# Kernel tuning notes

Measured on AMD Instinct MI355X. Metric: run time of the kernel, lower is better.

Reference implementation:

```python
import jax, jax.numpy as jnp
import numpy as np

STEPS = 2


def _gru_unit(adj, x, mask3, Wz0, Wz1, Wr0, Wr1, Wh0, Wh1, bz0, bz1, br0, br1, bh0, bh1):
    # adj: [B,N,N], x: [B,N,D], mask3: [B,N,1]
    a = jnp.einsum('bnm,bmd->bnd', adj, x)  # neighborhood aggregation
    z = jax.nn.sigmoid(a @ Wz0 + bz0 + x @ Wz1 + bz1)  # update gate
    r = jax.nn.sigmoid(a @ Wr0 + br0 + x @ Wr1 + br1)  # reset gate
    h = jax.nn.relu(mask3 * (a @ Wh0 + bh0 + (r * x) @ Wh1 + bh1))
    return h * z + x * (1.0 - z)


def setup_inputs() -> dict:
    key = jax.random.key(0)
    ks = jax.random.split(key, 10)
    B, N, Din, Dout = 256, 512, 300, 96

    def glorot(k, shape):
        lim = np.sqrt(6.0 / (shape[0] + shape[1]))
        return jax.random.uniform(k, shape, jnp.float32, -lim, lim)

    return {
        'x': jax.random.normal(ks[0], (B, N, Din), jnp.float32),
        'adj': jax.random.uniform(ks[1], (B, N, N), jnp.float32),
        'mask': jnp.ones((B, N), jnp.float32),
        'W_enc': glorot(ks[2], (Din, Dout)),
        'b_enc': jnp.zeros((Dout,), jnp.float32),
        'Wz0': glorot(ks[3], (Dout, Dout)),
        'Wz1': glorot(ks[4], (Dout, Dout)),
        'Wr0': glorot(ks[5], (Dout, Dout)),
        'Wr1': glorot(ks[6], (Dout, Dout)),
        'Wh0': glorot(ks[7], (Dout, Dout)),
        'Wh1': glorot(ks[8], (Dout, Dout)),
        'bz0': jnp.zeros((Dout,), jnp.float32),
        'bz1': jnp.zeros((Dout,), jnp.float32),
        'br0': jnp.zeros((Dout,), jnp.float32),
        'br1': jnp.zeros((Dout,), jnp.float32),
        'bh0': jnp.zeros((Dout,), jnp.float32),
        'bh1': jnp.zeros((Dout,), jnp.float32),
    }


def reference(x, adj, mask, W_enc, b_enc, Wz0, Wz1, Wr0, Wr1, Wh0, Wh1,
              bz0, bz1, br0, br1, bh0, bh1):
    mask3 = mask[..., None]                     # [B,N,1]
    xe = mask3 * jax.nn.relu(x)                 # dropout rate 0 -> identity
    out = xe @ W_enc + b_enc                    # [B,N,Dout]
    for _ in range(STEPS):
        out = _gru_unit(adj, out, mask3, Wz0, Wz1, Wr0, Wr1, Wh0, Wh1,
                        bz0, bz1, br0, br1, bh0, bh1)
    return out
```

## Files before the change

kernel.cpp:

```cpp
#include <hip/hip_runtime.h>

typedef short  bfrag  __attribute__((ext_vector_type(8)));
typedef float  facc4  __attribute__((ext_vector_type(4)));
typedef unsigned short u16;
typedef unsigned int   u32;

#define MROWS 131072
#define DD    96

__device__ __forceinline__ u16 f2b(float f) {
  u32 u = __float_as_uint(f);
  return (u16)((u + 0x7FFFu + ((u >> 16) & 1u)) >> 16);
}
__device__ __forceinline__ float b2f(u16 h) {
  return __uint_as_float(((u32)h) << 16);
}
__device__ __forceinline__ void splitf(float x, u16& h, u16& l) {
  h = f2b(x);
  l = f2b(x - b2f(h));
}
__device__ __forceinline__ void split4(float4 v, ushort4& oh, ushort4& ol) {
  splitf(v.x, oh.x, ol.x); splitf(v.y, oh.y, ol.y);
  splitf(v.z, oh.z, ol.z); splitf(v.w, oh.w, ol.w);
}

#define MFMA __builtin_amdgcn_mfma_f32_16x16x32_bf16

__global__ void k_prep(const float* __restrict__ Wenc,
                       const float* __restrict__ benc,
                       const float* __restrict__ Wz0, const float* __restrict__ Wz1,
                       const float* __restrict__ Wr0, const float* __restrict__ Wr1,
                       const float* __restrict__ Wh0, const float* __restrict__ Wh1,
                       const float* __restrict__ bz0, const float* __restrict__ bz1,
                       const float* __restrict__ br0, const float* __restrict__ br1,
                       const float* __restrict__ bh0, const float* __restrict__ bh1,
                       u16* __restrict__ wencTh, u16* __restrict__ wencTl,
                       u16* __restrict__ wzrTh,  u16* __restrict__ wzrTl,
                       u16* __restrict__ whTh,   u16* __restrict__ whTl,
                       float* __restrict__ bias)
{
  int i = blockIdx.x * 256 + threadIdx.x;
  if (i < 36864) {
    int n = i / 384, k = i % 384;
    float v = (k < 300) ? Wenc[k * 96 + n] : 0.f;
    u16 h, l; splitf(v, h, l);
    wencTh[i] = h; wencTl[i] = l;
  } else if (i < 73728) {
    int j = i - 36864;
    int g = j / 18432, r = j % 18432;
    int n = r / 192, k = r % 192;
    const float* W0 = g ? Wr0 : Wz0;
    const float* W1 = g ? Wr1 : Wz1;
    float v = (k < 96) ? W0[k * 96 + n] : W1[(k - 96) * 96 + n];
    u16 h, l; splitf(v, h, l);
    wzrTh[j] = h; wzrTl[j] = l;
  } else if (i < 92160) {
    int j = i - 73728;
    int n = j / 192, k = j % 192;
    float v = (k < 96) ? Wh0[k * 96 + n] : Wh1[(k - 96) * 96 + n];
    u16 h, l; splitf(v, h, l);
    whTh[j] = h; whTl[j] = l;
  } else if (i < 92544) {
    int j = i - 92160;
    int r = j / 96, n = j % 96;
    float v;
    if      (r == 0) v = benc[n];
    else if (r == 1) v = bz0[n] + bz1[n];
    else if (r == 2) v = br0[n] + br1[n];
    else             v = bh0[n] + bh1[n];
    bias[j] = v;
  }
}

__global__ __launch_bounds__(256) void k_enc(const float* __restrict__ x,
    const float* __restrict__ mask,
    const u16* __restrict__ wTh, const u16* __restrict__ wTl,
    const float* __restrict__ bias, float* __restrict__ xf)
{
  __shared__ u16 sAh[128][72], sAl[128][72];
  __shared__ u16 sBh[96][72],  sBl[96][72];
  const int tid = threadIdx.x;
  const int wave = tid >> 6, lane = tid & 63, q = lane >> 4, l15 = lane & 15;
  const int m0 = blockIdx.x * 128;
  facc4 acc[2][6] = {};
  for (int c = 0; c < 5; ++c) {
    int k0 = c * 64;
    {
      int rl = tid >> 2, cg = tid & 3;
      for (int it = 0; it < 2; ++it) {
        int row = rl + it * 64;
        int grow = m0 + row;
        float mk = mask[grow];
        const float* xr = x + (size_t)grow * 300 + k0;
        #pragma unroll
        for (int j = 0; j < 4; ++j) {
          int kk = (cg + j * 4) * 4;
          float4 v;
          if (k0 + kk + 4 <= 300) v = *(const float4*)(xr + kk);
          else                    v = make_float4(0.f, 0.f, 0.f, 0.f);
          v.x = fmaxf(v.x, 0.f) * mk; v.y = fmaxf(v.y, 0.f) * mk;
          v.z = fmaxf(v.z, 0.f) * mk; v.w = fmaxf(v.w, 0.f) * mk;
          ushort4 oh, ol; split4(v, oh, ol);
          *(ushort4*)&sAh[row][kk] = oh;
          *(ushort4*)&sAl[row][kk] = ol;
        }
      }
    }
    {
      for (int u = tid; u < 768; u += 256) {
        int n = u >> 3, kk = (u & 7) * 8;
        size_t off = (size_t)n * 384 + k0 + kk;
        *(uint4*)&sBh[n][kk] = *(const uint4*)(wTh + off);
        *(uint4*)&sBl[n][kk] = *(const uint4*)(wTl + off);
      }
    }
    __syncthreads();
    #pragma unroll
    for (int ks = 0; ks < 2; ++ks) {
      int kb = ks * 32 + q * 8;
      bfrag a0h = *(const bfrag*)&sAh[wave * 32 + l15][kb];
      bfrag a0l = *(const bfrag*)&sAl[wave * 32 + l15][kb];
      bfrag a1h = *(const bfrag*)&sAh[wave * 32 + 16 + l15][kb];
      bfrag a1l = *(const bfrag*)&sAl[wave * 32 + 16 + l15][kb];
      #pragma unroll
      for (int nt = 0; nt < 6; ++nt) {
        bfrag bh = *(const bfrag*)&sBh[nt * 16 + l15][kb];
        bfrag bl = *(const bfrag*)&sBl[nt * 16 + l15][kb];
        acc[0][nt] = MFMA(a0h, bh, acc[0][nt], 0, 0, 0);
        acc[0][nt] = MFMA(a0h, bl, acc[0][nt], 0, 0, 0);
        acc[0][nt] = MFMA(a0l, bh, acc[0][nt], 0, 0, 0);
        acc[1][nt] = MFMA(a1h, bh, acc[1][nt], 0, 0, 0);
        acc[1][nt] = MFMA(a1h, bl, acc[1][nt], 0, 0, 0);
        acc[1][nt] = MFMA(a1l, bh, acc[1][nt], 0, 0, 0);
      }
    }
    __syncthreads();
  }
  #pragma unroll
  for (int mt = 0; mt < 2; ++mt)
  #pragma unroll
  for (int rg = 0; rg < 4; ++rg) {
    int row = m0 + wave * 32 + mt * 16 + q * 4 + rg;
    #pragma unroll
    for (int nt = 0; nt < 6; ++nt) {
      int col = nt * 16 + l15;
      xf[(size_t)row * 96 + col] = acc[mt][nt][rg] + bias[col];
    }
  }
}

__global__ __launch_bounds__(256) void k_agg(const float* __restrict__ adj,
    const float* __restrict__ xf, float* af)
{
  __shared__ u16 sAh[128][72], sAl[128][72];
  __shared__ u16 sBh[96][72],  sBl[96][72];
  const int tid = threadIdx.x;
  const int wave = tid >> 6, lane = tid & 63, q = lane >> 4, l15 = lane & 15;
  const int bb = blockIdx.y;
  const int m0 = blockIdx.x * 128;
  const float* A = adj + (size_t)bb * 512 * 512;
  const float* X = xf  + (size_t)bb * 512 * 96;
  facc4 acc[2][6] = {};
  for (int c = 0; c < 8; ++c) {
    int k0 = c * 64;
    {
      int rl = tid >> 2, cg = tid & 3;
      for (int it = 0; it < 2; ++it) {
        int row = rl + it * 64;
        const float* ar_ = A + (size_t)(m0 + row) * 512 + k0;
        #pragma unroll
        for (int j = 0; j < 4; ++j) {
          int kk = (cg + j * 4) * 4;
          float4 v = *(const float4*)(ar_ + kk);
          ushort4 oh, ol; split4(v, oh, ol);
          *(ushort4*)&sAh[row][kk] = oh;
          *(ushort4*)&sAl[row][kk] = ol;
        }
      }
    }
    {
      int node = tid >> 2, seg = tid & 3;
      const float* xp = X + (size_t)(k0 + node) * 96;
      #pragma unroll
      for (int j = 0; j < 6; ++j) {
        int d = seg * 24 + j * 4;
        float4 v = *(const float4*)(xp + d);
        u16 h, l;
        splitf(v.x, h, l); sBh[d    ][node] = h; sBl[d    ][node] = l;
        splitf(v.y, h, l); sBh[d + 1][node] = h; sBl[d + 1][node] = l;
        splitf(v.z, h, l); sBh[d + 2][node] = h; sBl[d + 2][node] = l;
        splitf(v.w, h, l); sBh[d + 3][node] = h; sBl[d + 3][node] = l;
      }
    }
    __syncthreads();
    #pragma unroll
    for (int ks = 0; ks < 2; ++ks) {
      int kb = ks * 32 + q * 8;
      bfrag a0h = *(const bfrag*)&sAh[wave * 32 + l15][kb];
      bfrag a0l = *(const bfrag*)&sAl[wave * 32 + l15][kb];
      bfrag a1h = *(const bfrag*)&sAh[wave * 32 + 16 + l15][kb];
      bfrag a1l = *(const bfrag*)&sAl[wave * 32 + 16 + l15][kb];
      #pragma unroll
      for (int nt = 0; nt < 6; ++nt) {
        bfrag bh = *(const bfrag*)&sBh[nt * 16 + l15][kb];
        bfrag bl = *(const bfrag*)&sBl[nt * 16 + l15][kb];
        acc[0][nt] = MFMA(a0h, bh, acc[0][nt], 0, 0, 0);
        acc[0][nt] = MFMA(a0h, bl, acc[0][nt], 0, 0, 0);
        acc[0][nt] = MFMA(a0l, bh, acc[0][nt], 0, 0, 0);
        acc[1][nt] = MFMA(a1h, bh, acc[1][nt], 0, 0, 0);
        acc[1][nt] = MFMA(a1h, bl, acc[1][nt], 0, 0, 0);
        acc[1][nt] = MFMA(a1l, bh, acc[1][nt], 0, 0, 0);
      }
    }
    __syncthreads();
  }
  #pragma unroll
  for (int mt = 0; mt < 2; ++mt)
  #pragma unroll
  for (int rg = 0; rg < 4; ++rg) {
    int row = m0 + wave * 32 + mt * 16 + q * 4 + rg;
    size_t grow = (size_t)bb * 512 + row;
    #pragma unroll
    for (int nt = 0; nt < 6; ++nt) {
      int col = nt * 16 + l15;
      af[grow * 96 + col] = acc[mt][nt][rg];
    }
  }
}

__global__ __launch_bounds__(256) void k_gru(const float* af, float* xf,
    const u16* __restrict__ wzrTh, const u16* __restrict__ wzrTl,
    const u16* __restrict__ whTh,  const u16* __restrict__ whTl,
    const float* __restrict__ bias, const float* __restrict__ mask,
    float* outp, const int last)
{
  __shared__ u16 sAh[128][40],  sAl[128][40];
  __shared__ u16 sBzh[96][40],  sBzl[96][40];
  __shared__ u16 sBrh[96][40],  sBrl[96][40];
  __shared__ u16 sRxh[128][104], sRxl[128][104];
  const int tid = threadIdx.x;
  const int wave = tid >> 6, lane = tid & 63, q = lane >> 4, l15 = lane & 15;
  const int m0 = blockIdx.x * 128;

  facc4 az[2][6] = {}, ar[2][6] = {};
  for (int c = 0; c < 6; ++c) {
    const float* Asrc = (c < 3) ? af : xf;
    int ka = (c < 3 ? c : c - 3) * 32;
    {
      int row = tid >> 1, hf = tid & 1;
      const float* ap = Asrc + (size_t)(m0 + row) * 96 + ka + hf * 16;
      #pragma unroll
      for (int j = 0; j < 4; ++j) {
        int kk = hf * 16 + j * 4;
        float4 v = *(const float4*)(ap + j * 4);
        ushort4 oh, ol; split4(v, oh, ol);
        *(ushort4*)&sAh[row][kk] = oh;
        *(ushort4*)&sAl[row][kk] = ol;
      }
    }
    {
      int kw = c * 32;
      for (int u = tid; u < 384; u += 256) {
        int n = u >> 2, kk = (u & 3) * 8;
        size_t off = (size_t)n * 192 + kw + kk;
        *(uint4*)&sBzh[n][kk] = *(const uint4*)(wzrTh + off);
        *(uint4*)&sBzl[n][kk] = *(const uint4*)(wzrTl + off);
        *(uint4*)&sBrh[n][kk] = *(const uint4*)(wzrTh + 18432 + off);
        *(uint4*)&sBrl[n][kk] = *(const uint4*)(wzrTl + 18432 + off);
      }
    }
    __syncthreads();
    int kb = q * 8;
    bfrag a0h = *(const bfrag*)&sAh[wave * 32 + l15][kb];
    bfrag a0l = *(const bfrag*)&sAl[wave * 32 + l15][kb];
    bfrag a1h = *(const bfrag*)&sAh[wave * 32 + 16 + l15][kb];
    bfrag a1l = *(const bfrag*)&sAl[wave * 32 + 16 + l15][kb];
    #pragma unroll
    for (int nt = 0; nt < 6; ++nt) {
      bfrag bh = *(const bfrag*)&sBzh[nt * 16 + l15][kb];
      bfrag bl = *(const bfrag*)&sBzl[nt * 16 + l15][kb];
      az[0][nt] = MFMA(a0h, bh, az[0][nt], 0, 0, 0);
      az[0][nt] = MFMA(a0h, bl, az[0][nt], 0, 0, 0);
      az[0][nt] = MFMA(a0l, bh, az[0][nt], 0, 0, 0);
      az[1][nt] = MFMA(a1h, bh, az[1][nt], 0, 0, 0);
      az[1][nt] = MFMA(a1h, bl, az[1][nt], 0, 0, 0);
      az[1][nt] = MFMA(a1l, bh, az[1][nt], 0, 0, 0);
      bfrag ch = *(const bfrag*)&sBrh[nt * 16 + l15][kb];
      bfrag cl = *(const bfrag*)&sBrl[nt * 16 + l15][kb];
      ar[0][nt] = MFMA(a0h, ch, ar[0][nt], 0, 0, 0);
      ar[0][nt] = MFMA(a0h, cl, ar[0][nt], 0, 0, 0);
      ar[0][nt] = MFMA(a0l, ch, ar[0][nt], 0, 0, 0);
      ar[1][nt] = MFMA(a1h, ch, ar[1][nt], 0, 0, 0);
      ar[1][nt] = MFMA(a1h, cl, ar[1][nt], 0, 0, 0);
      ar[1][nt] = MFMA(a1l, ch, ar[1][nt], 0, 0, 0);
    }
    __syncthreads();
  }

  #pragma unroll
  for (int mt = 0; mt < 2; ++mt)
  #pragma unroll
  for (int rg = 0; rg < 4; ++rg) {
    int row = m0 + wave * 32 + mt * 16 + q * 4 + rg;
    #pragma unroll
    for (int nt = 0; nt < 6; ++nt) {
      int col = nt * 16 + l15;
      float vz = az[mt][nt][rg] + bias[96 + col];
      float vr = ar[mt][nt][rg] + bias[192 + col];
      float z = 1.f / (1.f + __expf(-vz));
      float r = 1.f / (1.f + __expf(-vr));
      az[mt][nt][rg] = z;
      float rx = r * xf[(size_t)row * 96 + col];
      u16 h, l; splitf(rx, h, l);
      sRxh[row - m0][col] = h;
      sRxl[row - m0][col] = l;
    }
  }
  __syncthreads();

  facc4 ah[2][6] = {};
  for (int c = 0; c < 6; ++c) {
    if (c < 3) {
      int row = tid >> 1, hf = tid & 1;
      const float* ap = af + (size_t)(m0 + row) * 96 + c * 32 + hf * 16;
      #pragma unroll
      for (int j = 0; j < 4; ++j) {
        int kk = hf * 16 + j * 4;
        float4 v = *(const float4*)(ap + j * 4);
        ushort4 oh, ol; split4(v, oh, ol);
        *(ushort4*)&sAh[row][kk] = oh;
        *(ushort4*)&sAl[row][kk] = ol;
      }
    }
    {
      int kw = c * 32;
      for (int u = tid; u < 384; u += 256) {
        int n = u >> 2, kk = (u & 3) * 8;
        size_t off = (size_t)n * 192 + kw + kk;
        *(uint4*)&sBzh[n][kk] = *(const uint4*)(whTh + off);
        *(uint4*)&sBzl[n][kk] = *(const uint4*)(whTl + off);
      }
    }
    __syncthreads();
    int kb = q * 8;
    bfrag a0h, a0l, a1h, a1l;
    if (c < 3) {
      a0h = *(const bfrag*)&sAh[wave * 32 + l15][kb];
      a0l = *(const bfrag*)&sAl[wave * 32 + l15][kb];
      a1h = *(const bfrag*)&sAh[wave * 32 + 16 + l15][kb];
      a1l = *(const bfrag*)&sAl[wave * 32 + 16 + l15][kb];
    } else {
      int ko = (c - 3) * 32 + kb;
      a0h = *(const bfrag*)&sRxh[wave * 32 + l15][ko];
      a0l = *(const bfrag*)&sRxl[wave * 32 + l15][ko];
      a1h = *(const bfrag*)&sRxh[wave * 32 + 16 + l15][ko];
      a1l = *(const bfrag*)&sRxl[wave * 32 + 16 + l15][ko];
    }
    #pragma unroll
    for (int nt = 0; nt < 6; ++nt) {
      bfrag bh = *(const bfrag*)&sBzh[nt * 16 + l15][kb];
      bfrag bl = *(const bfrag*)&sBzl[nt * 16 + l15][kb];
      ah[0][nt] = MFMA(a0h, bh, ah[0][nt], 0, 0, 0);
      ah[0][nt] = MFMA(a0h, bl, ah[0][nt], 0, 0, 0);
      ah[0][nt] = MFMA(a0l, bh, ah[0][nt], 0, 0, 0);
      ah[1][nt] = MFMA(a1h, bh, ah[1][nt], 0, 0, 0);
      ah[1][nt] = MFMA(a1h, bl, ah[1][nt], 0, 0, 0);
      ah[1][nt] = MFMA(a1l, bh, ah[1][nt], 0, 0, 0);
    }
    __syncthreads();
  }

  #pragma unroll
  for (int mt = 0; mt < 2; ++mt)
  #pragma unroll
  for (int rg = 0; rg < 4; ++rg) {
    int row = m0 + wave * 32 + mt * 16 + q * 4 + rg;
    float mk = mask[row];
    #pragma unroll
    for (int nt = 0; nt < 6; ++nt) {
      int col = nt * 16 + l15;
      size_t idx = (size_t)row * 96 + col;
      float pre = ah[mt][nt][rg] + bias[288 + col];
      float hv  = fmaxf(mk * pre, 0.f);
      float zv  = az[mt][nt][rg];
      float xv  = xf[idx];
      float o   = xv + zv * (hv - xv);
      if (last) outp[idx] = o;
      else      xf[idx]   = o;
    }
  }
}

extern "C" void kernel_launch(void* const* d_in, const int* in_sizes, int n_in,
                              void* d_out, int out_size, void* d_ws, size_t ws_size,
                              hipStream_t stream)
{
  const float* x    = (const float*)d_in[0];
  const float* adj  = (const float*)d_in[1];
  const float* mask = (const float*)d_in[2];
  const float* Wenc = (const float*)d_in[3];
  const float* benc = (const float*)d_in[4];
  const float* Wz0  = (const float*)d_in[5];
  const float* Wz1  = (const float*)d_in[6];
  const float* Wr0  = (const float*)d_in[7];
  const float* Wr1  = (const float*)d_in[8];
  const float* Wh0  = (const float*)d_in[9];
  const float* Wh1  = (const float*)d_in[10];
  const float* bz0  = (const float*)d_in[11];
  const float* bz1  = (const float*)d_in[12];
  const float* br0  = (const float*)d_in[13];
  const float* br1  = (const float*)d_in[14];
  const float* bh0  = (const float*)d_in[15];
  const float* bh1  = (const float*)d_in[16];

  char* ws = (char*)d_ws;
  const size_t NEL = (size_t)MROWS * DD;
  float* xf   = (float*)(ws);
  char*  wb   = ws + 4 * NEL;
  u16* wencTh = (u16*)(wb);
  u16* wencTl = (u16*)(wb + 73728);
  u16* wzrTh  = (u16*)(wb + 147456);
  u16* wzrTl  = (u16*)(wb + 221184);
  u16* whTh   = (u16*)(wb + 294912);
  u16* whTl   = (u16*)(wb + 331776);
  float* bias = (float*)(wb + 368640);

  float* af   = (float*)d_out;
  float* outp = (float*)d_out;

  k_prep<<<362, 256, 0, stream>>>(Wenc, benc, Wz0, Wz1, Wr0, Wr1, Wh0, Wh1,
                                  bz0, bz1, br0, br1, bh0, bh1,
                                  wencTh, wencTl, wzrTh, wzrTl, whTh, whTl, bias);
  k_enc<<<dim3(MROWS / 128), 256, 0, stream>>>(x, mask, wencTh, wencTl, bias, xf);
  for (int s = 0; s < 2; ++s) {
    int last = (s == 1);
    k_agg<<<dim3(4, 256), 256, 0, stream>>>(adj, xf, af);
    k_gru<<<dim3(MROWS / 128), 256, 0, stream>>>(af, xf, wzrTh, wzrTl, whTh, whTl,
                                                 bias, mask, outp, last);
  }
}
```

Measured before the change: 891.8 us.

## Register-prefetch and double-buffer GEMM tiles; fuse GRU aggregate passes

The encoder and aggregation kernels now issue the global loads for the next K-chunk into registers and write them into a second shared-memory buffer while MFMAs run on the current one, using smaller 32-wide K chunks. The transposed X tile in the aggregation kernel gets an XOR swizzle to cut LDS bank conflicts. In the GRU kernel, the a@Wh0 product now shares the first pass with the z/r gates, so af is read only once, and the remaining (r*x)@Wh1 pass prefetches its weights. Shared memory is aliased through a pool, and the extra syncs and register pressure may limit occupancy.

Result: slower. 929.1 us (+4.2%).

```diff
diff --git a/kernel.cpp b/kernel.cpp
--- a/kernel.cpp
+++ b/kernel.cpp
@@ -77,62 +77,84 @@
     const u16* __restrict__ wTh, const u16* __restrict__ wTl,
     const float* __restrict__ bias, float* __restrict__ xf)
 {
-  __shared__ u16 sAh[128][72], sAl[128][72];
-  __shared__ u16 sBh[96][72],  sBl[96][72];
+  __shared__ u16 sAh[2][128][40], sAl[2][128][40];
+  __shared__ u16 sBh[2][96][40],  sBl[2][96][40];
   const int tid = threadIdx.x;
   const int wave = tid >> 6, lane = tid & 63, q = lane >> 4, l15 = lane & 15;
   const int m0 = blockIdx.x * 128;
+  const int arow = tid >> 1, ahf = tid & 1;
+  const float mk = mask[m0 + arow];
+  const float* xrow = x + (size_t)(m0 + arow) * 300 + ahf * 16;
+
+  float4 Ra[4];
+  uint4  Rb[3];
+
+#define ENC_ISSUE_A(c) do { \
+    int kb0 = (c) * 32; \
+    _Pragma("unroll") \
+    for (int j = 0; j < 4; ++j) { \
+      int kk = kb0 + ahf * 16 + j * 4; \
+      if (kk + 4 <= 300) Ra[j] = *(const float4*)(xrow + kb0 + j * 4); \
+      else Ra[j] = make_float4(0.f, 0.f, 0.f, 0.f); \
+    } } while (0)
+
+#define ENC_ISSUE_B(c) do { \
+    _Pragma("unroll") \
+    for (int i = 0; i < 3; ++i) { \
+      int idx = tid + 256 * i; \
+      int half = idx >= 384; \
+      int rr = idx - half * 384; \
+      const u16* src = (half ? wTl : wTh) + (size_t)(rr >> 2) * 384 + (c) * 32 + (rr & 3) * 8; \
+      Rb[i] = *(const uint4*)src; \
+    } } while (0)
+
+#define ENC_WRITE(b) do { \
+    _Pragma("unroll") \
+    for (int j = 0; j < 4; ++j) { \
+      float4 v = Ra[j]; \
+      v.x = fmaxf(v.x, 0.f) * mk; v.y = fmaxf(v.y, 0.f) * mk; \
+      v.z = fmaxf(v.z, 0.f) * mk; v.w = fmaxf(v.w, 0.f) * mk; \
+      ushort4 oh, ol; split4(v, oh, ol); \
+      int kk = ahf * 16 + j * 4; \
+      *(ushort4*)&sAh[b][arow][kk] = oh; \
+      *(ushort4*)&sAl[b][arow][kk] = ol; \
+    } \
+    _Pragma("unroll") \
+    for (int i = 0; i < 3; ++i) { \
+      int idx = tid + 256 * i; \
+      int half = idx >= 384; \
+      int rr = idx - half * 384; \
+      int n = rr >> 2, sg = rr & 3; \
+      if (half) *(uint4*)&sBl[b][n][sg * 8] = Rb[i]; \
+      else      *(uint4*)&sBh[b][n][sg * 8] = Rb[i]; \
+    } } while (0)
+
   facc4 acc[2][6] = {};
-  for (int c = 0; c < 5; ++c) {
-    int k0 = c * 64;
-    {
-      int rl = tid >> 2, cg = tid & 3;
-      for (int it = 0; it < 2; ++it) {
-        int row = rl + it * 64;
-        int grow = m0 + row;
-        float mk = mask[grow];
-        const float* xr = x + (size_t)grow * 300 + k0;
-        #pragma unroll
-        for (int j = 0; j < 4; ++j) {
-          int kk = (cg + j * 4) * 4;
-          float4 v;
-          if (k0 + kk + 4 <= 300) v = *(const float4*)(xr + kk);
-          else                    v = make_float4(0.f, 0.f, 0.f, 0.f);
-          v.x = fmaxf(v.x, 0.f) * mk; v.y = fmaxf(v.y, 0.f) * mk;
-          v.z = fmaxf(v.z, 0.f) * mk; v.w = fmaxf(v.w, 0.f) * mk;
-          ushort4 oh, ol; split4(v, oh, ol);
-          *(ushort4*)&sAh[row][kk] = oh;
-          *(ushort4*)&sAl[row][kk] = ol;
-        }
-      }
-    }
-    {
-      for (int u = tid; u < 768; u += 256) {
-        int n = u >> 3, kk = (u & 7) * 8;
-        size_t off = (size_t)n * 384 + k0 + kk;
-        *(uint4*)&sBh[n][kk] = *(const uint4*)(wTh + off);
-        *(uint4*)&sBl[n][kk] = *(const uint4*)(wTl + off);
-      }
-    }
-    __syncthreads();
-    #pragma unroll
-    for (int ks = 0; ks < 2; ++ks) {
-      int kb = ks * 32 + q * 8;
-      bfrag a0h = *(const bfrag*)&sAh[wave * 32 + l15][kb];
-      bfrag a0l = *(const bfrag*)&sAl[wave * 32 + l15][kb];
-      bfrag a1h = *(const bfrag*)&sAh[wave * 32 + 16 + l15][kb];
-      bfrag a1l = *(const bfrag*)&sAl[wave * 32 + 16 + l15][kb];
-      #pragma unroll
-      for (int nt = 0; nt < 6; ++nt) {
-        bfrag bh = *(const bfrag*)&sBh[nt * 16 + l15][kb];
-        bfrag bl = *(const bfrag*)&sBl[nt * 16 + l15][kb];
-        acc[0][nt] = MFMA(a0h, bh, acc[0][nt], 0, 0, 0);
-        acc[0][nt] = MFMA(a0h, bl, acc[0][nt], 0, 0, 0);
-        acc[0][nt] = MFMA(a0l, bh, acc[0][nt], 0, 0, 0);
-        acc[1][nt] = MFMA(a1h, bh, acc[1][nt], 0, 0, 0);
-        acc[1][nt] = MFMA(a1h, bl, acc[1][nt], 0, 0, 0);
-        acc[1][nt] = MFMA(a1l, bh, acc[1][nt], 0, 0, 0);
-      }
+  ENC_ISSUE_A(0); ENC_ISSUE_B(0);
+  ENC_WRITE(0);
+  ENC_ISSUE_A(1); ENC_ISSUE_B(1);
+  __syncthreads();
+  for (int c = 0; c < 10; ++c) {
+    int cur = c & 1;
+    if (c < 9) {
+      ENC_WRITE(cur ^ 1);
+      if (c < 8) { ENC_ISSUE_A(c + 2); ENC_ISSUE_B(c + 2); }
+    }
+    int kb = q * 8;
+    bfrag a0h = *(const bfrag*)&sAh[cur][wave * 32 + l15][kb];
+    bfrag a0l = *(const bfrag*)&sAl[cur][wave * 32 + l15][kb];
+    bfrag a1h = *(const bfrag*)&sAh[cur][wave * 32 + 16 + l15][kb];
+    bfrag a1l = *(const bfrag*)&sAl[cur][wave * 32 + 16 + l15][kb];
+    #pragma unroll
+    for (int nt = 0; nt < 6; ++nt) {
+      bfrag bh = *(const bfrag*)&sBh[cur][nt * 16 + l15][kb];
+      bfrag bl = *(const bfrag*)&sBl[cur][nt * 16 + l15][kb];
+      acc[0][nt] = MFMA(a0h, bh, acc[0][nt], 0, 0, 0);
+      acc[0][nt] = MFMA(a0h, bl, acc[0][nt], 0, 0, 0);
+      acc[0][nt] = MFMA(a0l, bh, acc[0][nt], 0, 0, 0);
+      acc[1][nt] = MFMA(a1h, bh, acc[1][nt], 0, 0, 0);
+      acc[1][nt] = MFMA(a1h, bl, acc[1][nt], 0, 0, 0);
+      acc[1][nt] = MFMA(a1l, bh, acc[1][nt], 0, 0, 0);
     }
     __syncthreads();
   }
@@ -152,65 +174,75 @@
 __global__ __launch_bounds__(256) void k_agg(const float* __restrict__ adj,
     const float* __restrict__ xf, float* af)
 {
-  __shared__ u16 sAh[128][72], sAl[128][72];
-  __shared__ u16 sBh[96][72],  sBl[96][72];
+  __shared__ u16 sAh[2][128][40], sAl[2][128][40];
+  __shared__ u16 sBh[2][96][32],  sBl[2][96][32];
   const int tid = threadIdx.x;
   const int wave = tid >> 6, lane = tid & 63, q = lane >> 4, l15 = lane & 15;
   const int bb = blockIdx.y;
   const int m0 = blockIdx.x * 128;
   const float* A = adj + (size_t)bb * 512 * 512;
   const float* X = xf  + (size_t)bb * 512 * 96;
+  const int arow = tid >> 1, ahf = tid & 1;
+  const float* arp = A + (size_t)(m0 + arow) * 512 + ahf * 16;
+  const int bnode = tid >> 3, bseg = tid & 7;
+  const float* xp0 = X + (size_t)bnode * 96 + bseg * 12;
+
+  float4 Ra[4], Rb[3];
+
+#define AGG_ISSUE(c) do { \
+    const float* ap = arp + (c) * 32; \
+    _Pragma("unroll") for (int j = 0; j < 4; ++j) Ra[j] = *(const float4*)(ap + j * 4); \
+    const float* xp = xp0 + (size_t)(c) * 32 * 96; \
+    Rb[0] = *(const float4*)xp; \
+    Rb[1] = *(const float4*)(xp + 4); \
+    Rb[2] = *(const float4*)(xp + 8); } while (0)
+
+#define AGG_PUT(b, d, h, l) do { \
+    int off = (bnode * 2) ^ ((((d) >> 2) & 3) << 4); \
+    *(u16*)((char*)&sBh[b][d][0] + off) = (h); \
+    *(u16*)((char*)&sBl[b][d][0] + off) = (l); } while (0)
+
+#define AGG_WRITE(b) do { \
+    _Pragma("unroll") for (int j = 0; j < 4; ++j) { \
+      ushort4 oh, ol; split4(Ra[j], oh, ol); \
+      int kk = ahf * 16 + j * 4; \
+      *(ushort4*)&sAh[b][arow][kk] = oh; \
+      *(ushort4*)&sAl[b][arow][kk] = ol; } \
+    _Pragma("unroll") for (int i = 0; i < 3; ++i) { \
+      float4 v = Rb[i]; \
+      int d0 = bseg * 12 + i * 4; \
+      u16 h, l; \
+      splitf(v.x, h, l); AGG_PUT(b, d0    , h, l); \
+      splitf(v.y, h, l); AGG_PUT(b, d0 + 1, h, l); \
+      splitf(v.z, h, l); AGG_PUT(b, d0 + 2, h, l); \
+      splitf(v.w, h, l); AGG_PUT(b, d0 + 3, h, l); } } while (0)
+
   facc4 acc[2][6] = {};
-  for (int c = 0; c < 8; ++c) {
-    int k0 = c * 64;
-    {
-      int rl = tid >> 2, cg = tid & 3;
-      for (int it = 0; it < 2; ++it) {
-        int row = rl + it * 64;
-        const float* ar_ = A + (size_t)(m0 + row) * 512 + k0;
-        #pragma unroll
-        for (int j = 0; j < 4; ++j) {
-          int kk = (cg + j * 4) * 4;
-          float4 v = *(const float4*)(ar_ + kk);
-          ushort4 oh, ol; split4(v, oh, ol);
-          *(ushort4*)&sAh[row][kk] = oh;
-          *(ushort4*)&sAl[row][kk] = ol;
-        }
-      }
-    }
-    {
-      int node = tid >> 2, seg = tid & 3;
-      const float* xp = X + (size_t)(k0 + node) * 96;
-      #pragma unroll
-      for (int j = 0; j < 6; ++j) {
-        int d = seg * 24 + j * 4;
-        float4 v = *(const float4*)(xp + d);
-        u16 h, l;
-        splitf(v.x, h, l); sBh[d    ][node] = h; sBl[d    ][node] = l;
-        splitf(v.y, h, l); sBh[d + 1][node] = h; sBl[d + 1][node] = l;
-        splitf(v.z, h, l); sBh[d + 2][node] = h; sBl[d + 2][node] = l;
-        splitf(v.w, h, l); sBh[d + 3][node] = h; sBl[d + 3][node] = l;
-      }
-    }
-    __syncthreads();
-    #pragma unroll
-    for (int ks = 0; ks < 2; ++ks) {
-      int kb = ks * 32 + q * 8;
-      bfrag a0h = *(const bfrag*)&sAh[wave * 32 + l15][kb];
-      bfrag a0l = *(const bfrag*)&sAl[wave * 32 + l15][kb];
-      bfrag a1h = *(const bfrag*)&sAh[wave * 32 + 16 + l15][kb];
-      bfrag a1l = *(const bfrag*)&sAl[wave * 32 + 16 + l15][kb];
-      #pragma unroll
-      for (int nt = 0; nt < 6; ++nt) {
-        bfrag bh = *(const bfrag*)&sBh[nt * 16 + l15][kb];
-        bfrag bl = *(const bfrag*)&sBl[nt * 16 + l15][kb];
-        acc[0][nt] = MFMA(a0h, bh, acc[0][nt], 0, 0, 0);
-        acc[0][nt] = MFMA(a0h, bl, acc[0][nt], 0, 0, 0);
-        acc[0][nt] = MFMA(a0l, bh, acc[0][nt], 0, 0, 0);
-        acc[1][nt] = MFMA(a1h, bh, acc[1][nt], 0, 0, 0);
-        acc[1][nt] = MFMA(a1h, bl, acc[1][nt], 0, 0, 0);
-        acc[1][nt] = MFMA(a1l, bh, acc[1][nt], 0, 0, 0);
-      }
+  AGG_ISSUE(0); AGG_WRITE(0); AGG_ISSUE(1);
+  __syncthreads();
+  for (int c = 0; c < 16; ++c) {
+    int cur = c & 1;
+    if (c < 15) {
+      AGG_WRITE(cur ^ 1);
+      if (c < 14) AGG_ISSUE(c + 2);
+    }
+    int kb = q * 8;
+    bfrag a0h = *(const bfrag*)&sAh[cur][wave * 32 + l15][kb];
+    bfrag a0l = *(const bfrag*)&sAl[cur][wave * 32 + l15][kb];
+    bfrag a1h = *(const bfrag*)&sAh[cur][wave * 32 + 16 + l15][kb];
+    bfrag a1l = *(const bfrag*)&sAl[cur][wave * 32 + 16 + l15][kb];
+    #pragma unroll
+    for (int nt = 0; nt < 6; ++nt) {
+      int d = nt * 16 + l15;
+      int off = (q * 16) ^ (((d >> 2) & 3) << 4);
+      bfrag bh = *(const bfrag*)((const char*)&sBh[cur][d][0] + off);
+      bfrag bl = *(const bfrag*)((const char*)&sBl[cur][d][0] + off);
+      acc[0][nt] = MFMA(a0h, bh, acc[0][nt], 0, 0, 0);
+      acc[0][nt] = MFMA(a0h, bl, acc[0][nt], 0, 0, 0);
+      acc[0][nt] = MFMA(a0l, bh, acc[0][nt], 0, 0, 0);
+      acc[1][nt] = MFMA(a1h, bh, acc[1][nt], 0, 0, 0);
+      acc[1][nt] = MFMA(a1h, bl, acc[1][nt], 0, 0, 0);
+      acc[1][nt] = MFMA(a1l, bh, acc[1][nt], 0, 0, 0);
     }
     __syncthreads();
   }
@@ -234,42 +266,67 @@
     const float* __restrict__ bias, const float* __restrict__ mask,
     float* outp, const int last)
 {
-  __shared__ u16 sAh[128][40],  sAl[128][40];
-  __shared__ u16 sBzh[96][40],  sBzl[96][40];
-  __shared__ u16 sBrh[96][40],  sBrl[96][40];
-  __shared__ u16 sRxh[128][104], sRxl[128][104];
+  __shared__ __align__(16) char pool[68608];
+  u16 (*sAh)[40]   = (u16(*)[40])(pool);
+  u16 (*sAl)[40]   = (u16(*)[40])(pool + 10240);
+  u16 (*sBh)[40]   = (u16(*)[40])(pool + 20480);
+  u16 (*sBl)[40]   = (u16(*)[40])(pool + 43520);
+  u16 (*sRxh)[104] = (u16(*)[104])(pool);
+  u16 (*sRxl)[104] = (u16(*)[104])(pool + 26624);
+  u16 (*sB2h)[40]  = (u16(*)[40])(pool + 53248);
+  u16 (*sB2l)[40]  = (u16(*)[40])(pool + 60928);
+
   const int tid = threadIdx.x;
   const int wave = tid >> 6, lane = tid & 63, q = lane >> 4, l15 = lane & 15;
   const int m0 = blockIdx.x * 128;
-
-  facc4 az[2][6] = {}, ar[2][6] = {};
+  const int arow = tid >> 1, ahf = tid & 1;
+
+  float4 Ra[4];
+  uint4  Rz[3], Rr[3];
+
+#define GRU_ISSUE_A(c) do { \
+    const float* base = ((c) < 3 ? af : xf) + (size_t)(m0 + arow) * 96 + ((c) % 3) * 32 + ahf * 16; \
+    _Pragma("unroll") for (int j = 0; j < 4; ++j) Ra[j] = *(const float4*)(base + j * 4); \
+  } while (0)
+
+#define GRU_ISSUE_B(c) do { \
+    int kw = (c) * 32; \
+    _Pragma("unroll") for (int i = 0; i < 3; ++i) { \
+      int idx = tid + 256 * i; \
+      int half = idx >= 384; \
+      int rr = idx - half * 384; \
+      size_t o = (size_t)(rr >> 2) * 192 + kw + (rr & 3) * 8; \
+      const u16* sb = half ? wzrTl : wzrTh; \
+      Rz[i] = *(const uint4*)(sb + o); \
+      Rr[i] = *(const uint4*)(sb + 18432 + o); \
+    } } while (0)
+
+#define GRU_WRITE_1(kw, withH) do { \
+    _Pragma("unroll") for (int j = 0; j < 4; ++j) { \
+      ushort4 oh, ol; split4(Ra[j], oh, ol); \
+      int kk = ahf * 16 + j * 4; \
+      *(ushort4*)&sAh[arow][kk] = oh; \
+      *(ushort4*)&sAl[arow][kk] = ol; } \
+    _Pragma("unroll") for (int i = 0; i < 3; ++i) { \
+      int idx = tid + 256 * i; \
+      int half = idx >= 384; \
+      int rr = idx - half * 384; \
+      int n = rr >> 2, sg = rr & 3; \
+      if (half) { *(uint4*)&sBl[n][sg * 8] = Rz[i]; *(uint4*)&sBl[96 + n][sg * 8] = Rr[i]; } \
+      else      { *(uint4*)&sBh[n][sg * 8] = Rz[i]; *(uint4*)&sBh[96 + n][sg * 8] = Rr[i]; } \
+      if (withH) { \
+        size_t o = (size_t)n * 192 + (kw) + sg * 8; \
+        uint4 th = *(const uint4*)((half ? whTl : whTh) + o); \
+        if (half) *(uint4*)&sBl[192 + n][sg * 8] = th; \
+        else      *(uint4*)&sBh[192 + n][sg * 8] = th; \
+      } } } while (0)
+
+  facc4 az[2][6] = {}, ar[2][6] = {}, ah[2][6] = {};
+  GRU_ISSUE_A(0); GRU_ISSUE_B(0);
+  GRU_WRITE_1(0, 1);
+  __syncthreads();
   for (int c = 0; c < 6; ++c) {
-    const float* Asrc = (c < 3) ? af : xf;
-    int ka = (c < 3 ? c : c - 3) * 32;
-    {
-      int row = tid >> 1, hf = tid & 1;
-      const float* ap = Asrc + (size_t)(m0 + row) * 96 + ka + hf * 16;
-      #pragma unroll
-      for (int j = 0; j < 4; ++j) {
-        int kk = hf * 16 + j * 4;
-        float4 v = *(const float4*)(ap + j * 4);
-        ushort4 oh, ol; split4(v, oh, ol);
-        *(ushort4*)&sAh[row][kk] = oh;
-        *(ushort4*)&sAl[row][kk] = ol;
-      }
-    }
-    {
-      int kw = c * 32;
-      for (int u = tid; u < 384; u += 256) {
-        int n = u >> 2, kk = (u & 3) * 8;
-        size_t off = (size_t)n * 192 + kw + kk;
-        *(uint4*)&sBzh[n][kk] = *(const uint4*)(wzrTh + off);
-        *(uint4*)&sBzl[n][kk] = *(const uint4*)(wzrTl + off);
-        *(uint4*)&sBrh[n][kk] = *(const uint4*)(wzrTh + 18432 + off);
-        *(uint4*)&sBrl[n][kk] = *(const uint4*)(wzrTl + 18432 + off);
-      }
-    }
-    __syncthreads();
+    if (c < 5) { GRU_ISSUE_A(c + 1); GRU_ISSUE_B(c + 1); }
     int kb = q * 8;
     bfrag a0h = *(const bfrag*)&sAh[wave * 32 + l15][kb];
     bfrag a0l = *(const bfrag*)&sAl[wave * 32 + l15][kb];
@@ -277,16 +334,16 @@
     bfrag a1l = *(const bfrag*)&sAl[wave * 32 + 16 + l15][kb];
     #pragma unroll
     for (int nt = 0; nt < 6; ++nt) {
-      bfrag bh = *(const bfrag*)&sBzh[nt * 16 + l15][kb];
-      bfrag bl = *(const bfrag*)&sBzl[nt * 16 + l15][kb];
+      bfrag bh = *(const bfrag*)&sBh[nt * 16 + l15][kb];
+      bfrag bl = *(const bfrag*)&sBl[nt * 16 + l15][kb];
       az[0][nt] = MFMA(a0h, bh, az[0][nt], 0, 0, 0);
       az[0][nt] = MFMA(a0h, bl, az[0][nt], 0, 0, 0);
       az[0][nt] = MFMA(a0l, bh, az[0][nt], 0, 0, 0);
       az[1][nt] = MFMA(a1h, bh, az[1][nt], 0, 0, 0);
       az[1][nt] = MFMA(a1h, bl, az[1][nt], 0, 0, 0);
       az[1][nt] = MFMA(a1l, bh, az[1][nt], 0, 0, 0);
-      bfrag ch = *(const bfrag*)&sBrh[nt * 16 + l15][kb];
-      bfrag cl = *(const bfrag*)&sBrl[nt * 16 + l15][kb];
+      bfrag ch = *(const bfrag*)&sBh[96 + nt * 16 + l15][kb];
+      bfrag cl = *(const bfrag*)&sBl[96 + nt * 16 + l15][kb];
       ar[0][nt] = MFMA(a0h, ch, ar[0][nt], 0, 0, 0);
       ar[0][nt] = MFMA(a0h, cl, ar[0][nt], 0, 0, 0);
       ar[0][nt] = MFMA(a0l, ch, ar[0][nt], 0, 0, 0);
@@ -294,14 +351,29 @@
       ar[1][nt] = MFMA(a1h, cl, ar[1][nt], 0, 0, 0);
       ar[1][nt] = MFMA(a1l, ch, ar[1][nt], 0, 0, 0);
     }
+    if (c < 3) {
+      #pragma unroll
+      for (int nt = 0; nt < 6; ++nt) {
+        bfrag dh = *(const bfrag*)&sBh[192 + nt * 16 + l15][kb];
+        bfrag dl = *(const bfrag*)&sBl[192 + nt * 16 + l15][kb];
+        ah[0][nt] = MFMA(a0h, dh, ah[0][nt], 0, 0, 0);
+        ah[0][nt] = MFMA(a0h, dl, ah[0][nt], 0, 0, 0);
+        ah[0][nt] = MFMA(a0l, dh, ah[0][nt], 0, 0, 0);
+        ah[1][nt] = MFMA(a1h, dh, ah[1][nt], 0, 0, 0);
+        ah[1][nt] = MFMA(a1h, dl, ah[1][nt], 0, 0, 0);
+        ah[1][nt] = MFMA(a1l, dh, ah[1][nt], 0, 0, 0);
+      }
+    }
     __syncthreads();
+    if (c < 5) { GRU_WRITE_1((c + 1) * 32, (c + 1) < 3); __syncthreads(); }
   }
 
   #pragma unroll
   for (int mt = 0; mt < 2; ++mt)
   #pragma unroll
   for (int rg = 0; rg < 4; ++rg) {
-    int row = m0 + wave * 32 + mt * 16 + q * 4 + rg;
+    int row = wave * 32 + mt * 16 + q * 4 + rg;
+    int grow = m0 + row;
     #pragma unroll
     for (int nt = 0; nt < 6; ++nt) {
       int col = nt * 16 + l15;
@@ -310,56 +382,45 @@
       float z = 1.f / (1.f + __expf(-vz));
       float r = 1.f / (1.f + __expf(-vr));
       az[mt][nt][rg] = z;
-      float rx = r * xf[(size_t)row * 96 + col];
+      float rx = r * xf[(size_t)grow * 96 + col];
       u16 h, l; splitf(rx, h, l);
-      sRxh[row - m0][col] = h;
-      sRxl[row - m0][col] = l;
-    }
-  }
+      sRxh[row][col] = h;
+      sRxl[row][col] = l;
+    }
+  }
+
+  uint4 R2[3];
+#define GRU_ISSUE_B2(c) do { \
+    _Pragma("unroll") for (int i = 0; i < 3; ++i) { \
+      int idx = tid + 256 * i; \
+      int half = idx >= 384; \
+      int rr = idx - half * 384; \
+      size_t o = (size_t)(rr >> 2) * 192 + 96 + (c) * 32 + (rr & 3) * 8; \
+      R2[i] = *(const uint4*)((half ? whTl : whTh) + o); \
+    } } while (0)
+#define GRU_WRITE_B2() do { \
+    _Pragma("unroll") for (int i = 0; i < 3; ++i) { \
+      int idx = tid + 256 * i; \
+      int half = idx >= 384; \
+      int rr = idx - half * 384; \
+      int n = rr >> 2, sg = rr & 3; \
+      if (half) *(uint4*)&sB2l[n][sg * 8] = R2[i]; \
+      else      *(uint4*)&sB2h[n][sg * 8] = R2[i]; \
+    } } while (0)
+
+  GRU_ISSUE_B2(0); GRU_WRITE_B2();
   __syncthreads();
-
-  facc4 ah[2][6] = {};
-  for (int c = 0; c < 6; ++c) {
-    if (c < 3) {
-      int row = tid >> 1, hf = tid & 1;
-      const float* ap = af + (size_t)(m0 + row) * 96 + c * 32 + hf * 16;
-      #pragma unroll
-      for (int j = 0; j < 4; ++j) {
-        int kk = hf * 16 + j * 4;
-        float4 v = *(const float4*)(ap + j * 4);
-        ushort4 oh, ol; split4(v, oh, ol);
-        *(ushort4*)&sAh[row][kk] = oh;
-        *(ushort4*)&sAl[row][kk] = ol;
-      }
-    }
-    {
-      int kw = c * 32;
-      for (int u = tid; u < 384; u += 256) {
-        int n = u >> 2, kk = (u & 3) * 8;
-        size_t off = (size_t)n * 192 + kw + kk;
-        *(uint4*)&sBzh[n][kk] = *(const uint4*)(whTh + off);
-        *(uint4*)&sBzl[n][kk] = *(const uint4*)(whTl + off);
-      }
-    }
-    __syncthreads();
-    int kb = q * 8;
-    bfrag a0h, a0l, a1h, a1l;
-    if (c < 3) {
-      a0h = *(const bfrag*)&sAh[wave * 32 + l15][kb];
-      a0l = *(const bfrag*)&sAl[wave * 32 + l15][kb];
-      a1h = *(const bfrag*)&sAh[wave * 32 + 16 + l15][kb];
-      a1l = *(const bfrag*)&sAl[wave * 32 + 16 + l15][kb];
-    } else {
-      int ko = (c - 3) * 32 + kb;
-      a0h = *(const bfrag*)&sRxh[wave * 32 + l15][ko];
-      a0l = *(const bfrag*)&sRxl[wave * 32 + l15][ko];
-      a1h = *(const bfrag*)&sRxh[wave * 32 + 16 + l15][ko];
-      a1l = *(const bfrag*)&sRxl[wave * 32 + 16 + l15][ko];
-    }
-    #pragma unroll
-    for (int nt = 0; nt < 6; ++nt) {
-      bfrag bh = *(const bfrag*)&sBzh[nt * 16 + l15][kb];
-      bfrag bl = *(const bfrag*)&sBzl[nt * 16 + l15][kb];
+  for (int c = 0; c < 3; ++c) {
+    if (c < 2) GRU_ISSUE_B2(c + 1);
+    int kb = c * 32 + q * 8;
+    bfrag a0h = *(const bfrag*)&sRxh[wave * 32 + l15][kb];
+    bfrag a0l = *(const bfrag*)&sRxl[wave * 32 + l15][kb];
+    bfrag a1h = *(const bfrag*)&sRxh[wave * 32 + 16 + l15][kb];
+    bfrag a1l = *(const bfrag*)&sRxl[wave * 32 + 16 + l15][kb];
+    #pragma unroll
+    for (int nt = 0; nt < 6; ++nt) {
+      bfrag bh = *(const bfrag*)&sB2h[nt * 16 + l15][q * 8];
+      bfrag bl = *(const bfrag*)&sB2l[nt * 16 + l15][q * 8];
       ah[0][nt] = MFMA(a0h, bh, ah[0][nt], 0, 0, 0);
       ah[0][nt] = MFMA(a0h, bl, ah[0][nt], 0, 0, 0);
       ah[0][nt] = MFMA(a0l, bh, ah[0][nt], 0, 0, 0);
@@ -368,6 +429,7 @@
       ah[1][nt] = MFMA(a1l, bh, ah[1][nt], 0, 0, 0);
     }
     __syncthreads();
+    if (c < 2) { GRU_WRITE_B2(); __syncthreads(); }
   }
 
   #pragma unroll
```
